# Kernel optimization log

Measured on AMD Instinct MI355X. Metric: run time of the kernel, lower is better.

Reference implementation:

```python
import jax, jax.numpy as jnp
import numpy as np

B, S, T, V, D = 256, 256, 256, 512, 512


def _gru_cell(x, h, Wih, Whh, bih, bhh):
    # torch GRU semantics: gates ordered [r, z, n]
    gi = x @ Wih.T + bih            # [B, 3D]
    gh = h @ Whh.T + bhh            # [B, 3D]
    gi_r, gi_z, gi_n = jnp.split(gi, 3, axis=-1)
    gh_r, gh_z, gh_n = jnp.split(gh, 3, axis=-1)
    r = jax.nn.sigmoid(gi_r + gh_r)
    z = jax.nn.sigmoid(gi_z + gh_z)
    n = jnp.tanh(gi_n + r * gh_n)
    return (1.0 - z) * n + z * h


def setup_inputs() -> dict:
    key = jax.random.key(0)
    ks = jax.random.split(key, 14)
    s = 0.05
    inp = {
        "src": jax.random.randint(ks[0], (B, S), 0, V),
        "trg": jax.random.randint(ks[1], (B, T), 0, V),
        "src_mask": jnp.ones((B, S), dtype=bool),
        "trg_mask": jnp.ones((B, T), dtype=bool),
        "enc_emb": jax.random.normal(ks[2], (V, D), jnp.float32) * s,
        "enc_Wih": jax.random.normal(ks[3], (3 * D, D), jnp.float32) * s,
        "enc_Whh": jax.random.normal(ks[4], (3 * D, D), jnp.float32) * s,
        "enc_bih": jnp.zeros((3 * D,), jnp.float32),
        "enc_bhh": jnp.zeros((3 * D,), jnp.float32),
        "dec_emb": jax.random.normal(ks[5], (V, D), jnp.float32) * s,
        "dec_Wih": jax.random.normal(ks[6], (3 * D, D), jnp.float32) * s,
        "dec_Whh": jax.random.normal(ks[7], (3 * D, D), jnp.float32) * s,
        "dec_bih": jnp.zeros((3 * D,), jnp.float32),
        "dec_bhh": jnp.zeros((3 * D,), jnp.float32),
        "out_W": jax.random.normal(ks[8], (V, D), jnp.float32) * s,
        "out_b": jnp.zeros((V,), jnp.float32),
    }
    return inp


def reference(src, trg, src_mask, trg_mask,
              enc_emb, enc_Wih, enc_Whh, enc_bih, enc_bhh,
              dec_emb, dec_Wih, dec_Whh, dec_bih, dec_bhh,
              out_W, out_b):
    b = src.shape[0]
    d = enc_Whh.shape[1]

    # ---- encoder: embed (eval: no dropout) + GRU over src ----
    enc_x = enc_emb[src]                       # [B, S, D]
    h0 = jnp.zeros((b, d), enc_emb.dtype)

    def enc_step(h, x):
        return _gru_cell(x, h, enc_Wih, enc_Whh, enc_bih, enc_bhh), None

    h_enc, _ = jax.lax.scan(enc_step, h0, jnp.swapaxes(enc_x, 0, 1))

    # ---- decoder: relu(embed) + GRU step + linear per timestep ----
    dec_x = jax.nn.relu(dec_emb[trg])          # [B, T, D]

    def dec_step(h, x):
        h = _gru_cell(x, h, dec_Wih, dec_Whh, dec_bih, dec_bhh)
        logits = h @ out_W.T + out_b           # [B, V]
        return h, logits

    _, logits = jax.lax.scan(dec_step, h_enc, jnp.swapaxes(dec_x, 0, 1))
    logits = jnp.swapaxes(logits, 0, 1)        # [B, T, V]
    return jax.nn.log_softmax(logits, axis=-1)
```

## Files before the change

kernel.cpp:

```cpp
#include <hip/hip_runtime.h>
#include <cstdint>
#include <cstddef>

namespace {
constexpr int Dh = 512;
constexpr int G3 = 1536;
constexpr int NB = 256;
constexpr int SL = 256;
constexpr int TL = 256;
constexpr int NV = 512;
}

typedef __attribute__((ext_vector_type(8))) short bf16x8;
typedef __attribute__((ext_vector_type(4))) float f32x4;
typedef unsigned long long u64t;

__device__ __forceinline__ unsigned short f2bf(float f) {
  unsigned int u = __float_as_uint(f);
  u = (u + 0x7FFFu + ((u >> 16) & 1u)) >> 16;
  return (unsigned short)u;
}
__device__ __forceinline__ float bf2f(unsigned short s) {
  return __uint_as_float(((unsigned int)s) << 16);
}


__global__ __launch_bounds__(256) void cvt_bf16(const float* __restrict__ in,
                                                unsigned short* __restrict__ out,
                                                int n4, int relu) {
  int i = blockIdx.x * 256 + threadIdx.x;
  if (i >= n4) return;
  float4 v = ((const float4*)in)[i];
  if (relu) {
    v.x = fmaxf(v.x, 0.f); v.y = fmaxf(v.y, 0.f);
    v.z = fmaxf(v.z, 0.f); v.w = fmaxf(v.w, 0.f);
  }
  ushort4 o;
  o.x = f2bf(v.x); o.y = f2bf(v.y); o.z = f2bf(v.z); o.w = f2bf(v.w);
  ((ushort4*)out)[i] = o;
}

__global__ __launch_bounds__(256) void pack_whh(const unsigned short* __restrict__ Wb,
                                                unsigned short* __restrict__ Wpk) {
  const int idx = blockIdx.x * 256 + threadIdx.x;
  if (idx >= 16 * 6 * 16 * 64) return;
  const int dt = idx / 6144;
  const int rem = idx - dt * 6144;
  const int slot = rem >> 10;
  const int kk = (rem >> 6) & 15;
  const int l = rem & 63;
  const int n = slot / 3, g = slot - n * 3;
  const int row = g * 512 + dt * 32 + n * 16 + (l & 15);
  const int k = kk * 32 + (l >> 4) * 8;
  *(uint4*)(Wpk + (size_t)idx * 8) = *(const uint4*)(Wb + (size_t)row * Dh + k);
}

template <int AMODE, int OMODE>
__global__ __launch_bounds__(256) void gemm_bf16(
    const unsigned short* __restrict__ Abase, const int* __restrict__ idx,
    const unsigned short* __restrict__ W, const float* __restrict__ bias,
    void* __restrict__ Cout, int N) {
  __shared__ unsigned short lds_a[8 * 128 * 8];
  __shared__ unsigned short lds_b[8 * 128 * 8];
  const int t = threadIdx.x;
  const int n0 = blockIdx.x * 128;
  const int m0 = blockIdx.y * 128;
  const int w = t >> 6, l = t & 63;
  const int mq = (w & 1) * 64, nq = (w >> 1) * 64;
  const int l15 = l & 15, lh = l >> 4;

  const int sm = t & 127;
  const int sk = (t >> 7) * 4;
  const unsigned short* arow;
  if (AMODE == 0) {
    arow = Abase + (size_t)idx[m0 + sm] * Dh;
  } else {
    int row = m0 + sm;
    arow = Abase + ((size_t)(row & 255) * NB + (row >> 8)) * Dh;
  }
  const unsigned short* brow = W + (size_t)(n0 + sm) * Dh;

  f32x4 acc[4][4];
#pragma unroll
  for (int i = 0; i < 4; ++i)
#pragma unroll
    for (int j = 0; j < 4; ++j) acc[i][j] = (f32x4)0.f;

  for (int k0 = 0; k0 < Dh; k0 += 64) {
    __syncthreads();
#pragma unroll
    for (int i = 0; i < 4; ++i) {
      int kc = sk + i;
      *(uint4*)&lds_a[(kc * 128 + sm) * 8] = *(const uint4*)(arow + k0 + kc * 8);
      *(uint4*)&lds_b[(kc * 128 + sm) * 8] = *(const uint4*)(brow + k0 + kc * 8);
    }
    __syncthreads();
#pragma unroll
    for (int q = 0; q < 2; ++q) {
      bf16x8 af[4], bfr[4];
#pragma unroll
      for (int i = 0; i < 4; ++i)
        af[i] = *(const bf16x8*)&lds_a[((q * 4 + lh) * 128 + mq + i * 16 + l15) * 8];
#pragma unroll
      for (int j = 0; j < 4; ++j)
        bfr[j] = *(const bf16x8*)&lds_b[((q * 4 + lh) * 128 + nq + j * 16 + l15) * 8];
#pragma unroll
      for (int i = 0; i < 4; ++i)
#pragma unroll
        for (int j = 0; j < 4; ++j)
          acc[i][j] = __builtin_amdgcn_mfma_f32_16x16x32_bf16(af[i], bfr[j], acc[i][j], 0, 0, 0);
    }
  }

#pragma unroll
  for (int j = 0; j < 4; ++j) {
    const int col = n0 + nq + j * 16 + l15;
    const float bv = bias[col];
#pragma unroll
    for (int i = 0; i < 4; ++i) {
#pragma unroll
      for (int r = 0; r < 4; ++r) {
        const int row = m0 + mq + i * 16 + lh * 4 + r;
        const float v = acc[i][j][r] + bv;
        if (OMODE == 0) {
          ((float*)Cout)[(size_t)row * N + col] = v;
        } else {
          const int b = row >> 8, s = row & 255;
          const int g = col >> 9, d = col & 511;
          const int dt = d >> 5, nn_ = (d >> 4) & 1, cl = d & 15;
          ((unsigned short*)Cout)[((((size_t)s * NB + b) * 16 + dt) * 16 + cl) * 8 + nn_ * 3 + g] = f2bf(v);
        }
      }
    }
  }
}

__global__ __launch_bounds__(64, 1) void gru_persist2(
    const unsigned short* __restrict__ Wpk,
    const unsigned short* __restrict__ gi,
    const float* __restrict__ bhh,
    const float* __restrict__ h32_init,
    float* __restrict__ h32_final,
    unsigned short* __restrict__ hbA,
    unsigned short* __restrict__ hbB,
    unsigned short* __restrict__ hb_all,
    unsigned int* __restrict__ flags,
    int nsteps) {
  __shared__ unsigned short wl[6 * 16 * 64 * 8];
  const int wt = blockIdx.x;
  const int b0 = (wt >> 4) * 16;
  const int dt = wt & 15, d0 = dt * 32;
  const int l = threadIdx.x;
  const int l15 = l & 15, lh = l >> 4;

  {
    const uint4* wsrc = (const uint4*)(Wpk + (size_t)dt * 49152);
    uint4* wdst = (uint4*)wl;
#pragma unroll 4
    for (int i = 0; i < 96; ++i) wdst[i * 64 + l] = wsrc[i * 64 + l];
  }
  __syncthreads();

  float br_[2], bz_[2], bn_[2];
#pragma unroll
  for (int n = 0; n < 2; ++n) {
    const int d = d0 + n * 16 + l15;
    br_[n] = bhh[d]; bz_[n] = bhh[512 + d]; bn_[n] = bhh[1024 + d];
  }

  float hp[2][4];
#pragma unroll
  for (int n = 0; n < 2; ++n)
#pragma unroll
    for (int r = 0; r < 4; ++r)
      hp[n][r] = h32_init ? h32_init[(size_t)(b0 + lh * 4 + r) * Dh + d0 + n * 16 + l15] : 0.f;

  uint4 gpr[4];
#pragma unroll
  for (int r = 0; r < 4; ++r)
    gpr[r] = *(const uint4*)(gi + ((((size_t)0 * NB + b0 + lh * 4 + r) * 16 + dt) * 16 + l15) * 8);

  const unsigned int* fgrp = flags + (wt & ~15);

  for (int s = 0; s < nsteps; ++s) {
    const unsigned short* rdbuf;
    unsigned short* wrbuf;
    if (hb_all) {
      rdbuf = (s == 0) ? hbA : hb_all + (size_t)(s - 1) * NB * Dh;
      wrbuf = hb_all + (size_t)s * NB * Dh;
    } else {
      rdbuf = (s & 1) ? hbB : hbA;
      wrbuf = (s & 1) ? hbA : hbB;
    }

    if (s > 0) {
      const unsigned int tgt = (unsigned)s;
      unsigned int f;
      do {
        f = __hip_atomic_load(fgrp + l15, __ATOMIC_RELAXED, __HIP_MEMORY_SCOPE_SYSTEM);
        if (__all((int)(f >= tgt))) break;
        __builtin_amdgcn_s_sleep(1);
      } while (true);
      asm volatile("" ::: "memory");
    }

    const u64t* ap = (const u64t*)(rdbuf + (size_t)(b0 + l15) * Dh + lh * 8);
    bf16x8 af[16];
#pragma unroll
    for (int kk = 0; kk < 16; ++kk) {
      union { u64t q[2]; bf16x8 v; } u;
      u.q[0] = __hip_atomic_load(ap + kk * 8, __ATOMIC_RELAXED, __HIP_MEMORY_SCOPE_SYSTEM);
      u.q[1] = __hip_atomic_load(ap + kk * 8 + 1, __ATOMIC_RELAXED, __HIP_MEMORY_SCOPE_SYSTEM);
      af[kk] = u.v;
    }

    f32x4 acc[6];
#pragma unroll
    for (int sl_ = 0; sl_ < 6; ++sl_) acc[sl_] = (f32x4)0.f;
#pragma unroll
    for (int sl_ = 0; sl_ < 6; ++sl_)
#pragma unroll
      for (int kk = 0; kk < 16; ++kk) {
        bf16x8 bv = *(const bf16x8*)&wl[((sl_ * 16 + kk) * 64 + l) * 8];
        acc[sl_] = __builtin_amdgcn_mfma_f32_16x16x32_bf16(af[kk], bv, acc[sl_], 0, 0, 0);
      }

#pragma unroll
    for (int n = 0; n < 2; ++n)
#pragma unroll
      for (int r = 0; r < 4; ++r) {
        const unsigned short* gp = (const unsigned short*)&gpr[r];
        const float gir = bf2f(gp[n * 3 + 0]);
        const float giz = bf2f(gp[n * 3 + 1]);
        const float gin = bf2f(gp[n * 3 + 2]);
        const float rr = 1.f / (1.f + __expf(-(gir + acc[n * 3 + 0][r] + br_[n])));
        const float zz = 1.f / (1.f + __expf(-(giz + acc[n * 3 + 1][r] + bz_[n])));
        const float x2 = gin + rr * (acc[n * 3 + 2][r] + bn_[n]);
        const float nn = 1.f - 2.f / (__expf(2.f * x2) + 1.f);
        hp[n][r] = (1.f - zz) * nn + zz * hp[n][r];
      }

#pragma unroll
    for (int n = 0; n < 2; ++n)
#pragma unroll
      for (int r = 0; r < 4; ++r) {
        const float po = __shfl_xor(hp[n][r], 1, 64);
        if ((l15 & 1) == 0) {
          const unsigned int pk = (unsigned)f2bf(hp[n][r]) | ((unsigned)f2bf(po) << 16);
          const int b = b0 + lh * 4 + r, d = d0 + n * 16 + l15;
          __hip_atomic_store((unsigned int*)(wrbuf + (size_t)b * Dh + d), pk,
                             __ATOMIC_RELAXED, __HIP_MEMORY_SCOPE_SYSTEM);
        }
      }

    if (s + 1 < nsteps) {
      asm volatile("s_waitcnt vmcnt(0)" ::: "memory");
      if (l == 0)
        __hip_atomic_store(flags + wt, (unsigned)(s + 1), __ATOMIC_RELAXED,
                           __HIP_MEMORY_SCOPE_SYSTEM);
#pragma unroll
      for (int r = 0; r < 4; ++r)
        gpr[r] = *(const uint4*)(gi + ((((size_t)(s + 1) * NB + b0 + lh * 4 + r) * 16 + dt) * 16 + l15) * 8);
    }
  }

  if (h32_final) {
#pragma unroll
    for (int n = 0; n < 2; ++n)
#pragma unroll
      for (int r = 0; r < 4; ++r)
        h32_final[(size_t)(b0 + lh * 4 + r) * Dh + d0 + n * 16 + l15] = hp[n][r];
  }
}

__global__ __launch_bounds__(256) void logsoftmax512(float* __restrict__ x) {
  const int row = blockIdx.x * 4 + (threadIdx.x >> 6);
  const int lane = threadIdx.x & 63;
  float* p = x + (size_t)row * NV + lane * 8;
  float4 v0 = *(const float4*)p;
  float4 v1 = *(const float4*)(p + 4);
  float m = fmaxf(fmaxf(fmaxf(v0.x, v0.y), fmaxf(v0.z, v0.w)),
                  fmaxf(fmaxf(v1.x, v1.y), fmaxf(v1.z, v1.w)));
#pragma unroll
  for (int o = 1; o < 64; o <<= 1) m = fmaxf(m, __shfl_xor(m, o, 64));
  float s = expf(v0.x - m) + expf(v0.y - m) + expf(v0.z - m) + expf(v0.w - m) +
            expf(v1.x - m) + expf(v1.y - m) + expf(v1.z - m) + expf(v1.w - m);
#pragma unroll
  for (int o = 1; o < 64; o <<= 1) s += __shfl_xor(s, o, 64);
  const float ls = m + logf(s);
  v0.x -= ls; v0.y -= ls; v0.z -= ls; v0.w -= ls;
  v1.x -= ls; v1.y -= ls; v1.z -= ls; v1.w -= ls;
  *(float4*)p = v0;
  *(float4*)(p + 4) = v1;
}

extern "C" void kernel_launch(void* const* d_in, const int* in_sizes, int n_in,
                              void* d_out, int out_size, void* d_ws, size_t ws_size,
                              hipStream_t stream) {
  (void)in_sizes; (void)n_in; (void)out_size; (void)ws_size;
  const int* src = (const int*)d_in[0];
  const int* trg = (const int*)d_in[1];
  const float* enc_emb = (const float*)d_in[4];
  const float* enc_Wih = (const float*)d_in[5];
  const float* enc_Whh = (const float*)d_in[6];
  const float* enc_bih = (const float*)d_in[7];
  const float* enc_bhh = (const float*)d_in[8];
  const float* dec_emb = (const float*)d_in[9];
  const float* dec_Wih = (const float*)d_in[10];
  const float* dec_Whh = (const float*)d_in[11];
  const float* dec_bih = (const float*)d_in[12];
  const float* dec_bhh = (const float*)d_in[13];
  const float* out_W = (const float*)d_in[14];
  const float* out_b = (const float*)d_in[15];

  char* ws = (char*)d_ws;
  size_t off = 0;
  auto alloc = [&](size_t bytes) -> char* {
    char* p = ws + off;
    off += (bytes + 255) & ~(size_t)255;
    return p;
  };
  typedef unsigned short u16;
  u16* gi = (u16*)alloc((size_t)NB * SL * 16 * 16 * 8 * 2);
  u16* hb_all = (u16*)alloc((size_t)TL * NB * Dh * 2);
  float* h_enc = (float*)alloc((size_t)NB * Dh * 4);
  u16* hbA = (u16*)alloc((size_t)NB * Dh * 2);
  u16* hbB = (u16*)alloc((size_t)NB * Dh * 2);
  u16* embB_e = (u16*)alloc((size_t)NV * Dh * 2);
  u16* embB_d = (u16*)alloc((size_t)NV * Dh * 2);
  u16* WihB_e = (u16*)alloc((size_t)G3 * Dh * 2);
  u16* WhhB_e = (u16*)alloc((size_t)G3 * Dh * 2);
  u16* WihB_d = (u16*)alloc((size_t)G3 * Dh * 2);
  u16* WhhB_d = (u16*)alloc((size_t)G3 * Dh * 2);
  u16* outWB = (u16*)alloc((size_t)NV * Dh * 2);
  u16* Wpk_e = (u16*)alloc((size_t)16 * 6 * 16 * 64 * 8 * 2);
  u16* Wpk_d = (u16*)alloc((size_t)16 * 6 * 16 * 64 * 8 * 2);
  unsigned int* flags = (unsigned int*)alloc(2 * 256 * 4);

  cvt_bf16<<<(NV * Dh / 4 + 255) / 256, 256, 0, stream>>>(enc_emb, embB_e, NV * Dh / 4, 0);
  cvt_bf16<<<(NV * Dh / 4 + 255) / 256, 256, 0, stream>>>(dec_emb, embB_d, NV * Dh / 4, 1);
  cvt_bf16<<<(G3 * Dh / 4 + 255) / 256, 256, 0, stream>>>(enc_Wih, WihB_e, G3 * Dh / 4, 0);
  cvt_bf16<<<(G3 * Dh / 4 + 255) / 256, 256, 0, stream>>>(enc_Whh, WhhB_e, G3 * Dh / 4, 0);
  cvt_bf16<<<(G3 * Dh / 4 + 255) / 256, 256, 0, stream>>>(dec_Wih, WihB_d, G3 * Dh / 4, 0);
  cvt_bf16<<<(G3 * Dh / 4 + 255) / 256, 256, 0, stream>>>(dec_Whh, WhhB_d, G3 * Dh / 4, 0);
  cvt_bf16<<<(NV * Dh / 4 + 255) / 256, 256, 0, stream>>>(out_W, outWB, NV * Dh / 4, 0);
  pack_whh<<<384, 256, 0, stream>>>(WhhB_e, Wpk_e);
  pack_whh<<<384, 256, 0, stream>>>(WhhB_d, Wpk_d);
  hipMemsetAsync(hbA, 0, (size_t)NB * Dh * 2, stream);
  hipMemsetAsync(flags, 0, 2 * 256 * 4, stream);

  dim3 ggi(G3 / 128, NB * SL / 128);
  gemm_bf16<0, 2><<<ggi, 256, 0, stream>>>(embB_e, src, WihB_e, enc_bih, gi, G3);

  gru_persist2<<<dim3(256), 64, 0, stream>>>(Wpk_e, gi, enc_bhh, nullptr, h_enc,
                                             hbA, hbB, nullptr, flags, SL);

  gemm_bf16<0, 2><<<ggi, 256, 0, stream>>>(embB_d, trg, WihB_d, dec_bih, gi, G3);

  gru_persist2<<<dim3(256), 64, 0, stream>>>(Wpk_d, gi, dec_bhh, h_enc, nullptr,
                                             hbA, hbB, hb_all, flags + 256, TL);

  dim3 glg(NV / 128, NB * TL / 128);
  gemm_bf16<1, 0><<<glg, 256, 0, stream>>>(hb_all, nullptr, outWB, out_b, d_out, NV);
  logsoftmax512<<<NB * TL / 4, 256, 0, stream>>>((float*)d_out);
}
```

Baseline: 3.957 ms.

## Remap GRU workgroups so batch groups share an XCD and use agent-scope sync

```diff
diff --git a/kernel.cpp b/kernel.cpp
--- a/kernel.cpp
+++ b/kernel.cpp
@@ -22,6 +22,19 @@
 }
 __device__ __forceinline__ float bf2f(unsigned short s) {
   return __uint_as_float(((unsigned int)s) << 16);
+}
+
+__device__ __forceinline__ unsigned ld_u32(const unsigned* p, bool fast) {
+  return fast ? __hip_atomic_load(p, __ATOMIC_RELAXED, __HIP_MEMORY_SCOPE_AGENT)
+              : __hip_atomic_load(p, __ATOMIC_RELAXED, __HIP_MEMORY_SCOPE_SYSTEM);
+}
+__device__ __forceinline__ void st_u32(unsigned* p, unsigned v, bool fast) {
+  if (fast) __hip_atomic_store(p, v, __ATOMIC_RELAXED, __HIP_MEMORY_SCOPE_AGENT);
+  else      __hip_atomic_store(p, v, __ATOMIC_RELAXED, __HIP_MEMORY_SCOPE_SYSTEM);
+}
+__device__ __forceinline__ u64t ld_u64(const u64t* p, bool fast) {
+  return fast ? __hip_atomic_load(p, __ATOMIC_RELAXED, __HIP_MEMORY_SCOPE_AGENT)
+              : __hip_atomic_load(p, __ATOMIC_RELAXED, __HIP_MEMORY_SCOPE_SYSTEM);
 }
 
 
@@ -135,7 +148,7 @@
   }
 }
 
-__global__ __launch_bounds__(64, 1) void gru_persist2(
+__global__ __launch_bounds__(64, 1) void gru_persist3(
     const unsigned short* __restrict__ Wpk,
     const unsigned short* __restrict__ gi,
     const float* __restrict__ bhh,
@@ -145,13 +158,19 @@
     unsigned short* __restrict__ hbB,
     unsigned short* __restrict__ hb_all,
     unsigned int* __restrict__ flags,
+    unsigned int* __restrict__ xcdbuf,
     int nsteps) {
   __shared__ unsigned short wl[6 * 16 * 64 * 8];
   const int wt = blockIdx.x;
-  const int b0 = (wt >> 4) * 16;
-  const int dt = wt & 15, d0 = dt * 32;
+  const int grp = wt & 15;
+  const int dt = wt >> 4;
+  const int b0 = grp * 16;
+  const int d0 = dt * 32;
   const int l = threadIdx.x;
   const int l15 = l & 15, lh = l >> 4;
+
+  unsigned int* gflag = flags + grp * 16;
+  unsigned int* gxcd = xcdbuf + grp * 16;
 
   {
     const uint4* wsrc = (const uint4*)(Wpk + (size_t)dt * 49152);
@@ -159,6 +178,27 @@
 #pragma unroll 4
     for (int i = 0; i < 96; ++i) wdst[i * 64 + l] = wsrc[i * 64 + l];
   }
+
+  bool fast;
+  {
+    unsigned xcc;
+    asm("s_getreg_b32 %0, hwreg(HW_REG_XCC_ID)" : "=s"(xcc));
+    if (l == 0)
+      __hip_atomic_store(gxcd + dt, xcc + 1u, __ATOMIC_RELAXED, __HIP_MEMORY_SCOPE_SYSTEM);
+    asm volatile("s_waitcnt vmcnt(0)" ::: "memory");
+    if (l == 0)
+      __hip_atomic_store(gflag + dt, 1u, __ATOMIC_RELAXED, __HIP_MEMORY_SCOPE_SYSTEM);
+    unsigned f;
+    do {
+      f = __hip_atomic_load(gflag + l15, __ATOMIC_RELAXED, __HIP_MEMORY_SCOPE_SYSTEM);
+      if (__all((int)(f >= 1u))) break;
+      __builtin_amdgcn_s_sleep(1);
+    } while (true);
+    asm volatile("" ::: "memory");
+    unsigned x = __hip_atomic_load(gxcd + l15, __ATOMIC_RELAXED, __HIP_MEMORY_SCOPE_SYSTEM);
+    unsigned x0 = __shfl(x, 0, 64);
+    fast = (bool)__all((int)(x == x0));
+  }
   __syncthreads();
 
   float br_[2], bz_[2], bn_[2];
@@ -179,8 +219,6 @@
 #pragma unroll
   for (int r = 0; r < 4; ++r)
     gpr[r] = *(const uint4*)(gi + ((((size_t)0 * NB + b0 + lh * 4 + r) * 16 + dt) * 16 + l15) * 8);
-
-  const unsigned int* fgrp = flags + (wt & ~15);
 
   for (int s = 0; s < nsteps; ++s) {
     const unsigned short* rdbuf;
@@ -194,10 +232,10 @@
     }
 
     if (s > 0) {
-      const unsigned int tgt = (unsigned)s;
+      const unsigned int tgt = (unsigned)(s + 1);
       unsigned int f;
       do {
-        f = __hip_atomic_load(fgrp + l15, __ATOMIC_RELAXED, __HIP_MEMORY_SCOPE_SYSTEM);
+        f = ld_u32(gflag + l15, fast);
         if (__all((int)(f >= tgt))) break;
         __builtin_amdgcn_s_sleep(1);
       } while (true);
@@ -206,12 +244,22 @@
 
     const u64t* ap = (const u64t*)(rdbuf + (size_t)(b0 + l15) * Dh + lh * 8);
     bf16x8 af[16];
-#pragma unroll
-    for (int kk = 0; kk < 16; ++kk) {
-      union { u64t q[2]; bf16x8 v; } u;
-      u.q[0] = __hip_atomic_load(ap + kk * 8, __ATOMIC_RELAXED, __HIP_MEMORY_SCOPE_SYSTEM);
-      u.q[1] = __hip_atomic_load(ap + kk * 8 + 1, __ATOMIC_RELAXED, __HIP_MEMORY_SCOPE_SYSTEM);
-      af[kk] = u.v;
+    if (fast) {
+#pragma unroll
+      for (int kk = 0; kk < 16; ++kk) {
+        union { u64t q[2]; bf16x8 v; } u;
+        u.q[0] = __hip_atomic_load(ap + kk * 8, __ATOMIC_RELAXED, __HIP_MEMORY_SCOPE_AGENT);
+        u.q[1] = __hip_atomic_load(ap + kk * 8 + 1, __ATOMIC_RELAXED, __HIP_MEMORY_SCOPE_AGENT);
+        af[kk] = u.v;
+      }
+    } else {
+#pragma unroll
+      for (int kk = 0; kk < 16; ++kk) {
+        union { u64t q[2]; bf16x8 v; } u;
+        u.q[0] = __hip_atomic_load(ap + kk * 8, __ATOMIC_RELAXED, __HIP_MEMORY_SCOPE_SYSTEM);
+        u.q[1] = __hip_atomic_load(ap + kk * 8 + 1, __ATOMIC_RELAXED, __HIP_MEMORY_SCOPE_SYSTEM);
+        af[kk] = u.v;
+      }
     }
 
     f32x4 acc[6];
@@ -248,16 +296,13 @@
         if ((l15 & 1) == 0) {
           const unsigned int pk = (unsigned)f2bf(hp[n][r]) | ((unsigned)f2bf(po) << 16);
           const int b = b0 + lh * 4 + r, d = d0 + n * 16 + l15;
-          __hip_atomic_store((unsigned int*)(wrbuf + (size_t)b * Dh + d), pk,
-                             __ATOMIC_RELAXED, __HIP_MEMORY_SCOPE_SYSTEM);
+          st_u32((unsigned int*)(wrbuf + (size_t)b * Dh + d), pk, fast);
         }
       }
 
     if (s + 1 < nsteps) {
       asm volatile("s_waitcnt vmcnt(0)" ::: "memory");
-      if (l == 0)
-        __hip_atomic_store(flags + wt, (unsigned)(s + 1), __ATOMIC_RELAXED,
-                           __HIP_MEMORY_SCOPE_SYSTEM);
+      if (l == 0) st_u32(gflag + dt, (unsigned)(s + 2), fast);
 #pragma unroll
       for (int r = 0; r < 4; ++r)
         gpr[r] = *(const uint4*)(gi + ((((size_t)(s + 1) * NB + b0 + lh * 4 + r) * 16 + dt) * 16 + l15) * 8);
@@ -336,6 +381,7 @@
   u16* Wpk_e = (u16*)alloc((size_t)16 * 6 * 16 * 64 * 8 * 2);
   u16* Wpk_d = (u16*)alloc((size_t)16 * 6 * 16 * 64 * 8 * 2);
   unsigned int* flags = (unsigned int*)alloc(2 * 256 * 4);
+  unsigned int* xcdb = (unsigned int*)alloc(2 * 256 * 4);
 
   cvt_bf16<<<(NV * Dh / 4 + 255) / 256, 256, 0, stream>>>(enc_emb, embB_e, NV * Dh / 4, 0);
   cvt_bf16<<<(NV * Dh / 4 + 255) / 256, 256, 0, stream>>>(dec_emb, embB_d, NV * Dh / 4, 1);
@@ -348,17 +394,18 @@
   pack_whh<<<384, 256, 0, stream>>>(WhhB_d, Wpk_d);
   hipMemsetAsync(hbA, 0, (size_t)NB * Dh * 2, stream);
   hipMemsetAsync(flags, 0, 2 * 256 * 4, stream);
+  hipMemsetAsync(xcdb, 0, 2 * 256 * 4, stream);
 
   dim3 ggi(G3 / 128, NB * SL / 128);
   gemm_bf16<0, 2><<<ggi, 256, 0, stream>>>(embB_e, src, WihB_e, enc_bih, gi, G3);
 
-  gru_persist2<<<dim3(256), 64, 0, stream>>>(Wpk_e, gi, enc_bhh, nullptr, h_enc,
-                                             hbA, hbB, nullptr, flags, SL);
+  gru_persist3<<<dim3(256), 64, 0, stream>>>(Wpk_e, gi, enc_bhh, nullptr, h_enc,
+                                             hbA, hbB, nullptr, flags, xcdb, SL);
 
   gemm_bf16<0, 2><<<ggi, 256, 0, stream>>>(embB_d, trg, WihB_d, dec_bih, gi, G3);
 
-  gru_persist2<<<dim3(256), 64, 0, stream>>>(Wpk_d, gi, dec_bhh, h_enc, nullptr,
-                                             hbA, hbB, hb_all, flags + 256, TL);
+  gru_persist3<<<dim3(256), 64, 0, stream>>>(Wpk_d, gi, dec_bhh, h_enc, nullptr,
+                                             hbA, hbB, hb_all, flags + 256, xcdb + 256, TL);
 
   dim3 glg(NV / 128, NB * TL / 128);
   gemm_bf16<1, 0><<<glg, 256, 0, stream>>>(hb_all, nullptr, outWB, out_b, d_out, NV);
```

New measurement: 4.014 ms. No clear change (+1.4%).
